# Kernel tuning notes

Hardware: AMD Instinct MI355X
Metric: run time of the kernel (lower is better)

The kernel has to match this reference:

```python
import jax, jax.numpy as jnp
import numpy as np

D_MODEL = 1024
N_HEADS = 16
D_K = D_MODEL // N_HEADS


def setup_inputs() -> dict:
    key = jax.random.key(0)
    ks = jax.random.split(key, 5)
    s = 1.0 / np.sqrt(D_MODEL)  # mimic Linear init scale
    x = jax.random.normal(ks[0], (4, 2048, D_MODEL), dtype=jnp.float32)
    Wq = jax.random.normal(ks[1], (D_MODEL, D_MODEL), dtype=jnp.float32) * s
    Wk = jax.random.normal(ks[2], (D_MODEL, D_MODEL), dtype=jnp.float32) * s
    Wv = jax.random.normal(ks[3], (D_MODEL, D_MODEL), dtype=jnp.float32) * s
    Wo = jax.random.normal(ks[4], (D_MODEL, D_MODEL), dtype=jnp.float32) * s
    z = jnp.zeros((D_MODEL,), dtype=jnp.float32)
    return {"x": x, "Wq": Wq, "bq": z, "Wk": Wk, "bk": z, "Wv": Wv, "bv": z, "Wo": Wo, "bo": z}


def reference(x, Wq, bq, Wk, bk, Wv, bv, Wo, bo):
    B, S, _ = x.shape
    # Linear: y = x @ W^T + b (torch convention, W is [out, in])
    def proj(W, b):
        y = jnp.einsum('bsd,ed->bse', x, W) + b
        return y.reshape(B, S, N_HEADS, D_K).transpose(0, 2, 1, 3)  # [B,H,S,Dk]
    q = proj(Wq, bq)
    k = proj(Wk, bk)
    v = proj(Wv, bv)
    scale = 1.0 / np.sqrt(D_K)
    attn = jnp.einsum('bhqd,bhkd->bhqk', q, k) * scale  # [B,H,S,S]
    attn = jax.nn.softmax(attn, axis=-1)
    out = jnp.einsum('bhqk,bhkd->bhqd', attn, v)  # [B,H,S,Dk]
    out = out.transpose(0, 2, 1, 3).reshape(B, S, D_MODEL)
    return jnp.einsum('bsd,ed->bse', out, Wo) + bo
```

## Files before the change

### kernel.cpp

```cpp
#include <hip/hip_runtime.h>
#include <hip/hip_bf16.h>
#include <stdint.h>

#define DM   1024
#define NH   16
#define DKK  64
#define BB   4
#define SSEQ 2048
#define MTOT 8192

typedef __attribute__((ext_vector_type(8))) __bf16 bf16x8;
typedef __attribute__((ext_vector_type(4))) float f32x4;
typedef __attribute__((ext_vector_type(16))) float f32x16;
typedef __attribute__((ext_vector_type(4))) unsigned int u32x4;

__device__ __forceinline__ unsigned short f2bf(float f) {
  union { float f; unsigned int u; } v; v.f = f;
  unsigned int r = v.u + 0x7FFFu + ((v.u >> 16) & 1u);
  return (unsigned short)(r >> 16);
}

__device__ __forceinline__ unsigned int cvtpk(float lo, float hi) {
  unsigned int r;
  asm("v_cvt_pk_bf16_f32 %0, %1, %2" : "=v"(r) : "v"(lo), "v"(hi));
  return r;
}

__device__ __forceinline__ void gld16(const void* g, void* l) {
  typedef __attribute__((address_space(1))) const unsigned int gq_t;
  typedef __attribute__((address_space(3))) unsigned int lq_t;
  __builtin_amdgcn_global_load_lds((gq_t*)g, (lq_t*)l, 16, 0, 0);
}

__global__ __launch_bounds__(256)
void cast5(const float* __restrict__ x,  const float* __restrict__ wq,
           const float* __restrict__ wk, const float* __restrict__ wv,
           const float* __restrict__ wo,
           unsigned short* __restrict__ xb,  unsigned short* __restrict__ wqb,
           unsigned short* __restrict__ wkb, unsigned short* __restrict__ wvb,
           unsigned short* __restrict__ wob)
{
  const int blk = blockIdx.x;
  const float* src; unsigned short* dst; int base;
  if (blk < 512) { src = x; dst = xb; base = blk * 4096; }
  else {
    const int w = (blk - 512) >> 6, i = (blk - 512) & 63;
    base = i * 4096;
    src = (w==0) ? wq : (w==1) ? wk : (w==2) ? wv : wo;
    dst = (w==0) ? wqb : (w==1) ? wkb : (w==2) ? wvb : wob;
  }
  #pragma unroll
  for (int it = 0; it < 16; ++it) {
    const int idx = base + it*256 + (int)threadIdx.x;
    const float4 v = ((const float4*)src)[idx];
    ushort4 o; o.x = f2bf(v.x); o.y = f2bf(v.y); o.z = f2bf(v.z); o.w = f2bf(v.w);
    ((ushort4*)dst)[idx] = o;
  }
}

template<int MODE>
__global__ __launch_bounds__(256, 2)
void gemm_nt(const unsigned short* __restrict__ A,
             const unsigned short* __restrict__ Bw,
             const float* __restrict__ bias,
             void* __restrict__ Cp)
{
  __shared__ unsigned short As[128*32];
  __shared__ unsigned short Bs[128*32];
  int wg = blockIdx.x;
  wg = (wg & 7) * 64 + (wg >> 3);
  const int bm = wg >> 3, bn = wg & 7;
  const int m0 = bm * 128, n0 = bn * 128;
  const int tid = threadIdx.x;
  const int lane = tid & 63, wv = tid >> 6;
  const int wr = wv >> 1, wc = wv & 1;
  const int lr = lane & 15, lg = lane >> 4;

  const f32x4 fz = {0.f, 0.f, 0.f, 0.f};
  f32x4 acc[4][4];
  #pragma unroll
  for (int i = 0; i < 4; ++i)
    #pragma unroll
    for (int j = 0; j < 4; ++j) acc[i][j] = fz;

  const int srow = wv*16 + (lane >> 2);
  const int scol = (lane & 3) * 8;
  const unsigned short* Abase = A  + (size_t)(m0 + srow)*DM + scol;
  const unsigned short* Bbase = Bw + (size_t)(n0 + srow)*DM + scol;

  for (int kt = 0; kt < 32; ++kt) {
    const int kc = kt * 32;
    gld16(Abase + kc,          (char*)As + wv*1024);
    gld16(Abase + 64*DM + kc,  (char*)As + 4096 + wv*1024);
    gld16(Bbase + kc,          (char*)Bs + wv*1024);
    gld16(Bbase + 64*DM + kc,  (char*)Bs + 4096 + wv*1024);
    __syncthreads();
    bf16x8 af[4], bf[4];
    #pragma unroll
    for (int i = 0; i < 4; ++i)
      af[i] = *(const bf16x8*)&As[(wr*64 + i*16 + lr)*32 + lg*8];
    #pragma unroll
    for (int j = 0; j < 4; ++j)
      bf[j] = *(const bf16x8*)&Bs[(wc*64 + j*16 + lr)*32 + lg*8];
    #pragma unroll
    for (int i = 0; i < 4; ++i)
      #pragma unroll
      for (int j = 0; j < 4; ++j)
        acc[i][j] = __builtin_amdgcn_mfma_f32_16x16x32_bf16(af[i], bf[j], acc[i][j], 0, 0, 0);
    __syncthreads();
  }

  #pragma unroll
  for (int j = 0; j < 4; ++j) {
    const int n = n0 + wc*64 + j*16 + lr;
    const float bvv = bias[n];
    #pragma unroll
    for (int i = 0; i < 4; ++i) {
      #pragma unroll
      for (int r = 0; r < 4; ++r) {
        const int m = m0 + wr*64 + i*16 + lg*4 + r;
        float v = acc[i][j][r] + bvv;
        if (MODE == 3) v *= 0.18033688011112042f;
        if (MODE == 0 || MODE == 3) {
          const int b = m >> 11, s = m & 2047, h = n >> 6, d = n & 63;
          ((unsigned short*)Cp)[(size_t)((b*NH + h)*SSEQ + s)*DKK + d] = f2bf(v);
        } else if (MODE == 2) {
          const int b = m >> 11, s = m & 2047, h = n >> 6, d = n & 63;
          ((unsigned short*)Cp)[(size_t)(b*NH + h)*(SSEQ*DKK)
                                + (((s >> 4)*64 + d) << 4) + (s & 15)] = f2bf(v);
        } else {
          ((float*)Cp)[(size_t)m*DM + n] = v;
        }
      }
    }
  }
}

__device__ __forceinline__ u32x4 packP(const f32x16& s0, const f32x16& s1,
                                       const int ks, const int hi)
{
  const f32x16& sv = (ks < 2) ? s0 : s1;
  const int rb = (ks & 1) * 8;
  const unsigned int a0 = cvtpk(sv[rb+0], sv[rb+1]);
  const unsigned int a1 = cvtpk(sv[rb+2], sv[rb+3]);
  const unsigned int b0 = cvtpk(sv[rb+4], sv[rb+5]);
  const unsigned int b1 = cvtpk(sv[rb+6], sv[rb+7]);
  const unsigned int s0_ = hi ? a0 : b0;
  const unsigned int s1_ = hi ? a1 : b1;
  const unsigned int r0 = __shfl_xor(s0_, 32, 64);
  const unsigned int r1 = __shfl_xor(s1_, 32, 64);
  u32x4 pk;
  pk[0] = hi ? r0 : a0;
  pk[1] = hi ? r1 : a1;
  pk[2] = hi ? b0 : r0;
  pk[3] = hi ? b1 : r1;
  return pk;
}

__global__ __launch_bounds__(128, 2)
void attn2w(const unsigned short* __restrict__ Q,
            const unsigned short* __restrict__ K,
            const unsigned short* __restrict__ Vp,
            unsigned short* __restrict__ AO)
{
  __shared__ unsigned short Ks[2][4096];
  const int flat = blockIdx.x;
  const int xcd = flat & 7, idx = flat >> 3;
  const int bh = xcd*8 + (idx >> 4), qt = idx & 15;
  const int b = bh >> 4, h = bh & 15;
  const int tid = threadIdx.x, lane = tid & 63, wv = tid >> 6;
  const int l31 = lane & 31, hi = lane >> 5;
  const int qbase = qt*128 + wv*64;
  const size_t hoff = (size_t)bh * SSEQ * DKK;
  const unsigned short* Qg = Q  + hoff;
  const unsigned short* Kg = K  + hoff;
  const unsigned short* Vb = Vp + hoff;

  bf16x8 qfA[4], qfB[4];
  {
    const unsigned short* qrA = Qg + (size_t)(qbase + l31)*DKK + hi*8;
    const unsigned short* qrB = qrA + 32*DKK;
    #pragma unroll
    for (int ks = 0; ks < 4; ++ks) {
      qfA[ks] = *(const bf16x8*)(qrA + ks*16);
      qfB[ks] = *(const bf16x8*)(qrB + ks*16);
    }
  }

  f32x16 oA0, oA1, oB0, oB1;
  float laccA[8], laccB[8];
  #pragma unroll
  for (int r = 0; r < 16; ++r) { oA0[r]=0.f; oA1[r]=0.f; oB0[r]=0.f; oB1[r]=0.f; }
  #pragma unroll
  for (int r = 0; r < 8; ++r) { laccA[r]=0.f; laccB[r]=0.f; }

  const int sbase = wv*4096 + lane*16;
  const int cbyte = hi * 16;

  #define STAGE(bufi, kv0)                                                        \
    _Pragma("unroll")                                                             \
    for (int it = 0; it < 4; ++it) {                                              \
      const int LB  = sbase + it*1024;                                            \
      const int row = LB >> 7;                                                    \
      const int cb  = (LB & 127) ^ ((row & 7) << 4);                              \
      gld16(Kg + (size_t)((kv0) + row)*DKK + (cb >> 1),                           \
            (char*)&Ks[bufi][0] + LB);                                            \
    }

  STAGE(0, 0);
  __syncthreads();

  for (int kv = 0; kv < 32; ++kv) {
    const int buf = kv & 1;
    const int kv0 = kv * 64;

    bf16x8 vf0[4], vf1[4];
    {
      const unsigned short* vbase = Vb + (kv0 >> 4)*1024 + l31*16 + hi*8;
      #pragma unroll
      for (int ks = 0; ks < 4; ++ks) {
        vf0[ks] = *(const bf16x8*)(vbase + ks*1024);
        vf1[ks] = *(const bf16x8*)(vbase + ks*1024 + 512);
      }
    }

    if (kv < 31) { STAGE(buf ^ 1, kv0 + 64); }
    const char* KsB = (const char*)&Ks[buf][0];

    f32x16 sA0, sA1, sB0, sB1;
    #pragma unroll
    for (int r = 0; r < 16; ++r) { sA0[r]=0.f; sA1[r]=0.f; sB0[r]=0.f; sB1[r]=0.f; }
    __builtin_amdgcn_s_setprio(1);
    #pragma unroll
    for (int ks = 0; ks < 4; ++ks) {
      const int bo = l31*128 + ((ks*32 + cbyte) ^ ((l31 & 7) << 4));
      const bf16x8 kf0 = *(const bf16x8*)(KsB + bo);
      const bf16x8 kf1 = *(const bf16x8*)(KsB + bo + 4096);
      sA0 = __builtin_amdgcn_mfma_f32_32x32x16_bf16(kf0, qfA[ks], sA0, 0, 0, 0);
      sA1 = __builtin_amdgcn_mfma_f32_32x32x16_bf16(kf1, qfA[ks], sA1, 0, 0, 0);
      sB0 = __builtin_amdgcn_mfma_f32_32x32x16_bf16(kf0, qfB[ks], sB0, 0, 0, 0);
      sB1 = __builtin_amdgcn_mfma_f32_32x32x16_bf16(kf1, qfB[ks], sB1, 0, 0, 0);
    }
    __builtin_amdgcn_s_setprio(0);

    #pragma unroll
    for (int r = 0; r < 16; ++r) {
      sA0[r] = __builtin_amdgcn_exp2f(sA0[r]);
      sA1[r] = __builtin_amdgcn_exp2f(sA1[r]);
      sB0[r] = __builtin_amdgcn_exp2f(sB0[r]);
      sB1[r] = __builtin_amdgcn_exp2f(sB1[r]);
      laccA[r & 7] += sA0[r] + sA1[r];
      laccB[r & 7] += sB0[r] + sB1[r];
    }

    __builtin_amdgcn_s_setprio(1);
    #pragma unroll
    for (int ks = 0; ks < 4; ++ks) {
      const u32x4 pkA = packP(sA0, sA1, ks, hi);
      const u32x4 pkB = packP(sB0, sB1, ks, hi);
      const bf16x8 pbA = __builtin_bit_cast(bf16x8, pkA);
      const bf16x8 pbB = __builtin_bit_cast(bf16x8, pkB);
      oA0 = __builtin_amdgcn_mfma_f32_32x32x16_bf16(vf0[ks], pbA, oA0, 0, 0, 0);
      oA1 = __builtin_amdgcn_mfma_f32_32x32x16_bf16(vf1[ks], pbA, oA1, 0, 0, 0);
      oB0 = __builtin_amdgcn_mfma_f32_32x32x16_bf16(vf0[ks], pbB, oB0, 0, 0, 0);
      oB1 = __builtin_amdgcn_mfma_f32_32x32x16_bf16(vf1[ks], pbB, oB1, 0, 0, 0);
    }
    __builtin_amdgcn_s_setprio(0);
    __syncthreads();
  }

  float lA = ((laccA[0]+laccA[1])+(laccA[2]+laccA[3]))
           + ((laccA[4]+laccA[5])+(laccA[6]+laccA[7]));
  float lB = ((laccB[0]+laccB[1])+(laccB[2]+laccB[3]))
           + ((laccB[4]+laccB[5])+(laccB[6]+laccB[7]));
  lA += __shfl_xor(lA, 32, 64);
  lB += __shfl_xor(lB, 32, 64);
  const float invA = 1.f / lA, invB = 1.f / lB;

  char* lds = (char*)&Ks[0][0] + wv*8192;
  #pragma unroll
  for (int c = 0; c < 2; ++c) {
    const float inv = c ? invB : invA;
    const int row = c*32 + l31;
    const int swz = (l31 & 7) << 4;
    #pragma unroll
    for (int db = 0; db < 2; ++db) {
      const f32x16& o = c ? (db ? oB1 : oB0) : (db ? oA1 : oA0);
      #pragma unroll
      for (int r = 0; r < 16; r += 2) {
        const int d = db*32 + (r & 3) + 8*(r >> 2) + 4*hi;
        *(unsigned int*)(lds + row*128 + ((d*2) ^ swz)) = cvtpk(o[r]*inv, o[r+1]*inv);
      }
    }
  }
  __syncthreads();
  {
    const int q = qbase + lane - wv*64 + wv*64;
    unsigned short* orow = AO + (size_t)(b*SSEQ + (qt*128 + wv*64 + lane))*DM + h*DKK;
    (void)q;
    const int swz = (lane & 7) << 4;
    #pragma unroll
    for (int c16 = 0; c16 < 8; ++c16) {
      const uint4 v = *(const uint4*)(lds + lane*128 + ((c16*16) ^ swz));
      *(uint4*)(orow + c16*8) = v;
    }
  }
  #undef STAGE
}

extern "C" void kernel_launch(void* const* d_in, const int* in_sizes, int n_in,
                              void* d_out, int out_size, void* d_ws, size_t ws_size,
                              hipStream_t stream)
{
  (void)in_sizes; (void)n_in; (void)out_size; (void)ws_size;
  const float* x  = (const float*)d_in[0];
  const float* Wq = (const float*)d_in[1];
  const float* bq = (const float*)d_in[2];
  const float* Wk = (const float*)d_in[3];
  const float* bk = (const float*)d_in[4];
  const float* Wv = (const float*)d_in[5];
  const float* bv = (const float*)d_in[6];
  const float* Wo = (const float*)d_in[7];
  const float* bo = (const float*)d_in[8];

  char* ws = (char*)d_ws;
  unsigned short* xb  = (unsigned short*)(ws + 0);
  unsigned short* wqb = (unsigned short*)(ws + 16777216);
  unsigned short* wkb = (unsigned short*)(ws + 18874368);
  unsigned short* wvb = (unsigned short*)(ws + 20971520);
  unsigned short* wob = (unsigned short*)(ws + 23068672);
  unsigned short* Qb  = (unsigned short*)(ws + 25165824);
  unsigned short* Kb  = (unsigned short*)(ws + 41943040);
  unsigned short* Vpb = (unsigned short*)(ws + 58720256);
  unsigned short* AO  = xb;

  cast5<<<768, 256, 0, stream>>>(x, Wq, Wk, Wv, Wo, xb, wqb, wkb, wvb, wob);
  gemm_nt<3><<<512, 256, 0, stream>>>(xb, wqb, bq, Qb);
  gemm_nt<0><<<512, 256, 0, stream>>>(xb, wkb, bk, Kb);
  gemm_nt<2><<<512, 256, 0, stream>>>(xb, wvb, bv, Vpb);
  attn2w<<<1024, 128, 0, stream>>>(Qb, Kb, Vpb, AO);
  gemm_nt<1><<<512, 256, 0, stream>>>(AO, wob, bo, (float*)d_out);
}
```

Measured before the change: 198.3 us.

## Fuse QKV GEMMs into one launch and halve attention query tile per block

The three separate Q/K/V projection launches become one 1536-block kernel that selects its weight, bias and output layout from the block index. The attention kernel now gives each wave 32 query rows instead of 64, doubling the grid to 2048 blocks and raising the occupancy hint to 4 blocks per CU. The goals are to cut launch gaps and tail effects between the GEMMs and to give attention more parallelism and latency hiding. The cost is that each K tile staged into LDS and each V fragment loaded is reused across half as many queries, so K/V traffic per unit of work roughly doubles.

```diff
diff --git a/kernel.cpp b/kernel.cpp
--- a/kernel.cpp
+++ b/kernel.cpp
@@ -58,12 +58,94 @@
   }
 }
 
-template<int MODE>
 __global__ __launch_bounds__(256, 2)
-void gemm_nt(const unsigned short* __restrict__ A,
-             const unsigned short* __restrict__ Bw,
-             const float* __restrict__ bias,
-             void* __restrict__ Cp)
+void gemm_qkv(const unsigned short* __restrict__ A,
+              const unsigned short* __restrict__ wqb,
+              const unsigned short* __restrict__ wkb,
+              const unsigned short* __restrict__ wvb,
+              const float* __restrict__ bq, const float* __restrict__ bk,
+              const float* __restrict__ bv,
+              unsigned short* __restrict__ Qb, unsigned short* __restrict__ Kb,
+              unsigned short* __restrict__ Vpb)
+{
+  __shared__ unsigned short As[128*32];
+  __shared__ unsigned short Bs[128*32];
+  const int blk = blockIdx.x;
+  const int wg = (blk & 7) * 192 + (blk >> 3);
+  const int bm = wg / 24, bnv = wg % 24;
+  const int w = bnv >> 3, bn = bnv & 7;
+  const int m0 = bm * 128, n0 = bn * 128;
+  const unsigned short* Bw   = (w==0) ? wqb : (w==1) ? wkb : wvb;
+  const float*          bias = (w==0) ? bq  : (w==1) ? bk  : bv;
+  const int tid = threadIdx.x;
+  const int lane = tid & 63, wv = tid >> 6;
+  const int wr = wv >> 1, wc = wv & 1;
+  const int lr = lane & 15, lg = lane >> 4;
+
+  const f32x4 fz = {0.f, 0.f, 0.f, 0.f};
+  f32x4 acc[4][4];
+  #pragma unroll
+  for (int i = 0; i < 4; ++i)
+    #pragma unroll
+    for (int j = 0; j < 4; ++j) acc[i][j] = fz;
+
+  const int srow = wv*16 + (lane >> 2);
+  const int scol = (lane & 3) * 8;
+  const unsigned short* Abase = A  + (size_t)(m0 + srow)*DM + scol;
+  const unsigned short* Bbase = Bw + (size_t)(n0 + srow)*DM + scol;
+
+  for (int kt = 0; kt < 32; ++kt) {
+    const int kc = kt * 32;
+    gld16(Abase + kc,          (char*)As + wv*1024);
+    gld16(Abase + 64*DM + kc,  (char*)As + 4096 + wv*1024);
+    gld16(Bbase + kc,          (char*)Bs + wv*1024);
+    gld16(Bbase + 64*DM + kc,  (char*)Bs + 4096 + wv*1024);
+    __syncthreads();
+    bf16x8 af[4], bf[4];
+    #pragma unroll
+    for (int i = 0; i < 4; ++i)
+      af[i] = *(const bf16x8*)&As[(wr*64 + i*16 + lr)*32 + lg*8];
+    #pragma unroll
+    for (int j = 0; j < 4; ++j)
+      bf[j] = *(const bf16x8*)&Bs[(wc*64 + j*16 + lr)*32 + lg*8];
+    #pragma unroll
+    for (int i = 0; i < 4; ++i)
+      #pragma unroll
+      for (int j = 0; j < 4; ++j)
+        acc[i][j] = __builtin_amdgcn_mfma_f32_16x16x32_bf16(af[i], bf[j], acc[i][j], 0, 0, 0);
+    __syncthreads();
+  }
+
+  #pragma unroll
+  for (int j = 0; j < 4; ++j) {
+    const int n = n0 + wc*64 + j*16 + lr;
+    const float bvv = bias[n];
+    #pragma unroll
+    for (int i = 0; i < 4; ++i) {
+      #pragma unroll
+      for (int r = 0; r < 4; ++r) {
+        const int m = m0 + wr*64 + i*16 + lg*4 + r;
+        float v = acc[i][j][r] + bvv;
+        const int b = m >> 11, s = m & 2047, h = n >> 6, d = n & 63;
+        if (w == 0) {
+          v *= 0.18033688011112042f;
+          Qb[(size_t)((b*NH + h)*SSEQ + s)*DKK + d] = f2bf(v);
+        } else if (w == 1) {
+          Kb[(size_t)((b*NH + h)*SSEQ + s)*DKK + d] = f2bf(v);
+        } else {
+          Vpb[(size_t)(b*NH + h)*(SSEQ*DKK)
+              + (((s >> 4)*64 + d) << 4) + (s & 15)] = f2bf(v);
+        }
+      }
+    }
+  }
+}
+
+__global__ __launch_bounds__(256, 2)
+void gemm_out(const unsigned short* __restrict__ A,
+              const unsigned short* __restrict__ Bw,
+              const float* __restrict__ bias,
+              float* __restrict__ Cp)
 {
   __shared__ unsigned short As[128*32];
   __shared__ unsigned short Bs[128*32];
@@ -119,18 +201,7 @@
       #pragma unroll
       for (int r = 0; r < 4; ++r) {
         const int m = m0 + wr*64 + i*16 + lg*4 + r;
-        float v = acc[i][j][r] + bvv;
-        if (MODE == 3) v *= 0.18033688011112042f;
-        if (MODE == 0 || MODE == 3) {
-          const int b = m >> 11, s = m & 2047, h = n >> 6, d = n & 63;
-          ((unsigned short*)Cp)[(size_t)((b*NH + h)*SSEQ + s)*DKK + d] = f2bf(v);
-        } else if (MODE == 2) {
-          const int b = m >> 11, s = m & 2047, h = n >> 6, d = n & 63;
-          ((unsigned short*)Cp)[(size_t)(b*NH + h)*(SSEQ*DKK)
-                                + (((s >> 4)*64 + d) << 4) + (s & 15)] = f2bf(v);
-        } else {
-          ((float*)Cp)[(size_t)m*DM + n] = v;
-        }
+        Cp[(size_t)m*DM + n] = acc[i][j][r] + bvv;
       }
     }
   }
@@ -157,8 +228,8 @@
   return pk;
 }
 
-__global__ __launch_bounds__(128, 2)
-void attn2w(const unsigned short* __restrict__ Q,
+__global__ __launch_bounds__(128, 4)
+void attn1c(const unsigned short* __restrict__ Q,
             const unsigned short* __restrict__ K,
             const unsigned short* __restrict__ Vp,
             unsigned short* __restrict__ AO)
@@ -166,33 +237,30 @@
   __shared__ unsigned short Ks[2][4096];
   const int flat = blockIdx.x;
   const int xcd = flat & 7, idx = flat >> 3;
-  const int bh = xcd*8 + (idx >> 4), qt = idx & 15;
+  const int bh = xcd*8 + (idx >> 5), qt = idx & 31;
   const int b = bh >> 4, h = bh & 15;
   const int tid = threadIdx.x, lane = tid & 63, wv = tid >> 6;
   const int l31 = lane & 31, hi = lane >> 5;
-  const int qbase = qt*128 + wv*64;
+  const int q0 = qt*64 + wv*32;
   const size_t hoff = (size_t)bh * SSEQ * DKK;
   const unsigned short* Qg = Q  + hoff;
   const unsigned short* Kg = K  + hoff;
   const unsigned short* Vb = Vp + hoff;
 
-  bf16x8 qfA[4], qfB[4];
+  bf16x8 qf[4];
   {
-    const unsigned short* qrA = Qg + (size_t)(qbase + l31)*DKK + hi*8;
-    const unsigned short* qrB = qrA + 32*DKK;
-    #pragma unroll
-    for (int ks = 0; ks < 4; ++ks) {
-      qfA[ks] = *(const bf16x8*)(qrA + ks*16);
-      qfB[ks] = *(const bf16x8*)(qrB + ks*16);
-    }
-  }
-
-  f32x16 oA0, oA1, oB0, oB1;
-  float laccA[8], laccB[8];
-  #pragma unroll
-  for (int r = 0; r < 16; ++r) { oA0[r]=0.f; oA1[r]=0.f; oB0[r]=0.f; oB1[r]=0.f; }
-  #pragma unroll
-  for (int r = 0; r < 8; ++r) { laccA[r]=0.f; laccB[r]=0.f; }
+    const unsigned short* qr = Qg + (size_t)(q0 + l31)*DKK + hi*8;
+    #pragma unroll
+    for (int ks = 0; ks < 4; ++ks)
+      qf[ks] = *(const bf16x8*)(qr + ks*16);
+  }
+
+  f32x16 oA0, oA1;
+  float lacc[8];
+  #pragma unroll
+  for (int r = 0; r < 16; ++r) { oA0[r]=0.f; oA1[r]=0.f; }
+  #pragma unroll
+  for (int r = 0; r < 8; ++r) lacc[r] = 0.f;
 
   const int sbase = wv*4096 + lane*16;
   const int cbyte = hi * 16;
@@ -227,65 +295,51 @@
     if (kv < 31) { STAGE(buf ^ 1, kv0 + 64); }
     const char* KsB = (const char*)&Ks[buf][0];
 
-    f32x16 sA0, sA1, sB0, sB1;
-    #pragma unroll
-    for (int r = 0; r < 16; ++r) { sA0[r]=0.f; sA1[r]=0.f; sB0[r]=0.f; sB1[r]=0.f; }
+    f32x16 s0, s1;
+    #pragma unroll
+    for (int r = 0; r < 16; ++r) { s0[r]=0.f; s1[r]=0.f; }
     __builtin_amdgcn_s_setprio(1);
     #pragma unroll
     for (int ks = 0; ks < 4; ++ks) {
       const int bo = l31*128 + ((ks*32 + cbyte) ^ ((l31 & 7) << 4));
       const bf16x8 kf0 = *(const bf16x8*)(KsB + bo);
       const bf16x8 kf1 = *(const bf16x8*)(KsB + bo + 4096);
-      sA0 = __builtin_amdgcn_mfma_f32_32x32x16_bf16(kf0, qfA[ks], sA0, 0, 0, 0);
-      sA1 = __builtin_amdgcn_mfma_f32_32x32x16_bf16(kf1, qfA[ks], sA1, 0, 0, 0);
-      sB0 = __builtin_amdgcn_mfma_f32_32x32x16_bf16(kf0, qfB[ks], sB0, 0, 0, 0);
-      sB1 = __builtin_amdgcn_mfma_f32_32x32x16_bf16(kf1, qfB[ks], sB1, 0, 0, 0);
+      s0 = __builtin_amdgcn_mfma_f32_32x32x16_bf16(kf0, qf[ks], s0, 0, 0, 0);
+      s1 = __builtin_amdgcn_mfma_f32_32x32x16_bf16(kf1, qf[ks], s1, 0, 0, 0);
     }
     __builtin_amdgcn_s_setprio(0);
 
     #pragma unroll
     for (int r = 0; r < 16; ++r) {
-      sA0[r] = __builtin_amdgcn_exp2f(sA0[r]);
-      sA1[r] = __builtin_amdgcn_exp2f(sA1[r]);
-      sB0[r] = __builtin_amdgcn_exp2f(sB0[r]);
-      sB1[r] = __builtin_amdgcn_exp2f(sB1[r]);
-      laccA[r & 7] += sA0[r] + sA1[r];
-      laccB[r & 7] += sB0[r] + sB1[r];
+      s0[r] = __builtin_amdgcn_exp2f(s0[r]);
+      s1[r] = __builtin_amdgcn_exp2f(s1[r]);
+      lacc[r & 7] += s0[r] + s1[r];
     }
 
     __builtin_amdgcn_s_setprio(1);
     #pragma unroll
     for (int ks = 0; ks < 4; ++ks) {
-      const u32x4 pkA = packP(sA0, sA1, ks, hi);
-      const u32x4 pkB = packP(sB0, sB1, ks, hi);
-      const bf16x8 pbA = __builtin_bit_cast(bf16x8, pkA);
-      const bf16x8 pbB = __builtin_bit_cast(bf16x8, pkB);
-      oA0 = __builtin_amdgcn_mfma_f32_32x32x16_bf16(vf0[ks], pbA, oA0, 0, 0, 0);
-      oA1 = __builtin_amdgcn_mfma_f32_32x32x16_bf16(vf1[ks], pbA, oA1, 0, 0, 0);
-      oB0 = __builtin_amdgcn_mfma_f32_32x32x16_bf16(vf0[ks], pbB, oB0, 0, 0, 0);
-      oB1 = __builtin_amdgcn_mfma_f32_32x32x16_bf16(vf1[ks], pbB, oB1, 0, 0, 0);
+      const u32x4 pk = packP(s0, s1, ks, hi);
+      const bf16x8 pb = __builtin_bit_cast(bf16x8, pk);
+      oA0 = __builtin_amdgcn_mfma_f32_32x32x16_bf16(vf0[ks], pb, oA0, 0, 0, 0);
+      oA1 = __builtin_amdgcn_mfma_f32_32x32x16_bf16(vf1[ks], pb, oA1, 0, 0, 0);
     }
     __builtin_amdgcn_s_setprio(0);
     __syncthreads();
   }
 
-  float lA = ((laccA[0]+laccA[1])+(laccA[2]+laccA[3]))
-           + ((laccA[4]+laccA[5])+(laccA[6]+laccA[7]));
-  float lB = ((laccB[0]+laccB[1])+(laccB[2]+laccB[3]))
-           + ((laccB[4]+laccB[5])+(laccB[6]+laccB[7]));
+  float lA = ((lacc[0]+lacc[1])+(lacc[2]+lacc[3]))
+           + ((lacc[4]+lacc[5])+(lacc[6]+lacc[7]));
   lA += __shfl_xor(lA, 32, 64);
-  lB += __shfl_xor(lB, 32, 64);
-  const float invA = 1.f / lA, invB = 1.f / lB;
-
-  char* lds = (char*)&Ks[0][0] + wv*8192;
-  #pragma unroll
-  for (int c = 0; c < 2; ++c) {
-    const float inv = c ? invB : invA;
-    const int row = c*32 + l31;
+  const float inv = 1.f / lA;
+
+  char* lds = (char*)&Ks[0][0] + wv*4096;
+  {
+    const int row = l31;
     const int swz = (l31 & 7) << 4;
     #pragma unroll
     for (int db = 0; db < 2; ++db) {
-      const f32x16& o = c ? (db ? oB1 : oB0) : (db ? oA1 : oA0);
+      const f32x16& o = db ? oA1 : oA0;
       #pragma unroll
       for (int r = 0; r < 16; r += 2) {
         const int d = db*32 + (r & 3) + 8*(r >> 2) + 4*hi;
@@ -295,13 +349,13 @@
   }
   __syncthreads();
   {
-    const int q = qbase + lane - wv*64 + wv*64;
-    unsigned short* orow = AO + (size_t)(b*SSEQ + (qt*128 + wv*64 + lane))*DM + h*DKK;
-    (void)q;
-    const int swz = (lane & 7) << 4;
-    #pragma unroll
-    for (int c16 = 0; c16 < 8; ++c16) {
-      const uint4 v = *(const uint4*)(lds + lane*128 + ((c16*16) ^ swz));
+    const int q = q0 + l31;
+    unsigned short* orow = AO + (size_t)(b*SSEQ + q)*DM + h*DKK;
+    const int swz = (l31 & 7) << 4;
+    #pragma unroll
+    for (int it = 0; it < 4; ++it) {
+      const int c16 = hi + 2*it;
+      const uint4 v = *(const uint4*)(lds + l31*128 + ((c16*16) ^ swz));
       *(uint4*)(orow + c16*8) = v;
     }
   }
@@ -335,9 +389,7 @@
   unsigned short* AO  = xb;
 
   cast5<<<768, 256, 0, stream>>>(x, Wq, Wk, Wv, Wo, xb, wqb, wkb, wvb, wob);
-  gemm_nt<3><<<512, 256, 0, stream>>>(xb, wqb, bq, Qb);
-  gemm_nt<0><<<512, 256, 0, stream>>>(xb, wkb, bk, Kb);
-  gemm_nt<2><<<512, 256, 0, stream>>>(xb, wvb, bv, Vpb);
-  attn2w<<<1024, 128, 0, stream>>>(Qb, Kb, Vpb, AO);
-  gemm_nt<1><<<512, 256, 0, stream>>>(AO, wob, bo, (float*)d_out);
-}
+  gemm_qkv<<<1536, 256, 0, stream>>>(xb, wqb, wkb, wvb, bq, bk, bv, Qb, Kb, Vpb);
+  attn1c<<<2048, 128, 0, stream>>>(Qb, Kb, Vpb, AO);
+  gemm_out<<<512, 256, 0, stream>>>(AO, wob, bo, (float*)d_out);
+}
```

Result: slower. 272.9 us (+37.6%).
